# Performance work log

Hardware: AMD Instinct MI355X
Metric: run time of the kernel (lower is better)

## Reference

```python
import math
import jax, jax.numpy as jnp
from jax import lax
import numpy as np

LN_EPS = 1e-5
K = 3          # deform-conv kernel size
PAD = 1        # 'same' padding so offset map matches output resolution


def setup_inputs() -> dict:
    key = jax.random.key(0)
    ks = jax.random.split(key, 6)
    B, C, H, W, Co = 4, 256, 64, 64, 256
    x = jax.random.normal(ks[0], (B, C, H, W), jnp.float32)
    dwc_w = jax.random.normal(ks[1], (C, 1, K, K), jnp.float32) * 0.02
    ln_w = jnp.ones((C,), jnp.float32)
    ln_b = jnp.zeros((C,), jnp.float32)
    fcd_w = jax.random.normal(ks[2], (1, C, 1, 1), jnp.float32) * 0.02
    fca_w = jax.random.normal(ks[3], (1, C, 1, 1), jnp.float32) * 0.02
    fan_in = C * K * K
    dconv_w = jax.random.normal(ks[4], (Co, C, K, K), jnp.float32) / math.sqrt(fan_in)
    dconv_b = jnp.zeros((Co,), jnp.float32)
    return dict(x=x, dwc_w=dwc_w, ln_w=ln_w, ln_b=ln_b,
                fcd_w=fcd_w, fca_w=fca_w, dconv_w=dconv_w, dconv_b=dconv_b)


def _bilinear_sample(x, py, px):
    # x: [B,C,H,W]; py/px: [B,KK,H,W] float sample positions (zero-padded border)
    B, C, H, W = x.shape
    y0 = jnp.floor(py); x0 = jnp.floor(px)
    y1 = y0 + 1.0;      x1 = x0 + 1.0
    wy1 = py - y0; wy0 = 1.0 - wy1
    wx1 = px - x0; wx0 = 1.0 - wx1

    def gather(yy, xx):
        valid = ((yy >= 0) & (yy < H) & (xx >= 0) & (xx < W)).astype(x.dtype)
        iy = jnp.clip(yy, 0, H - 1).astype(jnp.int32)
        ix = jnp.clip(xx, 0, W - 1).astype(jnp.int32)
        # per-batch fancy gather -> [B,C,KK,H,W]
        v = jax.vmap(lambda img, a, b: img[:, a, b])(x, iy, ix)
        return v * valid[:, None]

    return (gather(y0, x0) * (wy0 * wx0)[:, None]
          + gather(y0, x1) * (wy0 * wx1)[:, None]
          + gather(y1, x0) * (wy1 * wx0)[:, None]
          + gather(y1, x1) * (wy1 * wx1)[:, None])


def reference(x, dwc_w, ln_w, ln_b, fcd_w, fca_w, dconv_w, dconv_b):
    B, C, H, W = x.shape
    KK = K * K
    # --- offset branch ---
    h = lax.conv_general_dilated(x, dwc_w, (1, 1), ((1, 1), (1, 1)),
                                 dimension_numbers=('NCHW', 'OIHW', 'NCHW'),
                                 feature_group_count=C)
    mu = h.mean(axis=1, keepdims=True)
    var = h.var(axis=1, keepdims=True)
    h = (h - mu) * lax.rsqrt(var + LN_EPS)
    h = h * ln_w[None, :, None, None] + ln_b[None, :, None, None]
    h = jax.nn.relu(h)
    r = jax.nn.relu(jnp.einsum('bchw,oc->bohw', h, fcd_w[:, :, 0, 0]))      # [B,1,H,W]
    t = jnp.einsum('bchw,oc->bohw', h, fca_w[:, :, 0, 0])
    theta = (t / (1.0 + jnp.abs(t))) * (math.pi / 180.0)                     # softsign * pi/180
    ox = r * jnp.cos(theta)
    oy = r * jnp.sin(theta)
    # torch code: offsets = cat([ox tiled KK, oy tiled KK], dim=1) -> [B,2KK,H,W]
    off = jnp.concatenate([jnp.tile(ox, (1, KK, 1, 1)), jnp.tile(oy, (1, KK, 1, 1))], axis=1)
    # torchvision DeformConv2d convention: channel 2k = dy, channel 2k+1 = dx
    dy = off[:, 0::2]   # [B,KK,H,W]
    dx = off[:, 1::2]
    # --- deformable sampling ---
    ky = jnp.repeat(jnp.arange(K), K).astype(x.dtype)   # kernel row per tap
    kx = jnp.tile(jnp.arange(K), K).astype(x.dtype)     # kernel col per tap
    py = (jnp.arange(H, dtype=x.dtype) - PAD)[None, None, :, None] + ky[None, :, None, None] + dy
    px = (jnp.arange(W, dtype=x.dtype) - PAD)[None, None, None, :] + kx[None, :, None, None] + dx
    sampled = _bilinear_sample(x, py, px)               # [B,C,KK,H,W]
    Co = dconv_w.shape[0]
    out = jnp.einsum('bckhw,ock->bohw', sampled, dconv_w.reshape(Co, C, KK))
    return out + dconv_b[None, :, None, None]
```

## Files before the change

### kernel.cpp

```cpp
#include <hip/hip_runtime.h>
#include <hip/hip_bf16.h>

#define B_   4
#define C_   256
#define CO_  256
#define H_   64
#define W_   64
#define HW_  4096

typedef __attribute__((ext_vector_type(8))) short short8;
typedef __attribute__((ext_vector_type(4))) float f32x4;
typedef __attribute__((ext_vector_type(2))) float f32x2;

static __device__ __forceinline__ unsigned short f2bf(float f) {
    unsigned u = __builtin_bit_cast(unsigned, f);
    unsigned r = (u + 0x7fffu + ((u >> 16) & 1u)) >> 16;
    return (unsigned short)r;
}
static __device__ __forceinline__ f32x2 pk_mul(f32x2 a, f32x2 b) {
    f32x2 d; asm("v_pk_mul_f32 %0, %1, %2" : "=v"(d) : "v"(a), "v"(b)); return d;
}
static __device__ __forceinline__ f32x2 pk_fma(f32x2 a, f32x2 b, f32x2 c) {
    f32x2 d; asm("v_pk_fma_f32 %0, %1, %2, %3" : "=v"(d) : "v"(a), "v"(b), "v"(c)); return d;
}
static __device__ __forceinline__ f32x2 pk_add(f32x2 a, f32x2 b) {
    f32x2 d; asm("v_pk_add_f32 %0, %1, %2" : "=v"(d) : "v"(a), "v"(b)); return d;
}
static __device__ __forceinline__ unsigned cvtpk(float a, float b) {
    unsigned r; asm("v_cvt_pk_bf16_f32 %0, %1, %2" : "=v"(r) : "v"(a), "v"(b)); return r;
}
static __device__ __forceinline__ f32x2 unpack_bf2(unsigned d) {
    f32x2 v;
    v.x = __builtin_bit_cast(float, d << 16);
    v.y = __builtin_bit_cast(float, d & 0xffff0000u);
    return v;
}

__global__ void k_pre(const float* __restrict__ x, unsigned short* __restrict__ xT,
                      const float* __restrict__ w, unsigned short* __restrict__ Bt,
                      const float* __restrict__ dwc_w, float* __restrict__ dwcT)
{
    int bid = blockIdx.x;
    int tid = threadIdx.x;
    if (bid < 1024) {
        __shared__ float t[32][132];
        int b   = bid >> 8;
        int rem = bid & 255;
        int hwT = rem >> 1, cT = rem & 1;
        int hw0 = hwT * 32, c0 = cT * 128;
        const float* src = x + (size_t)b * C_ * HW_;
        {
            int hw4 = (tid & 7) << 2;
            int cr  = tid >> 3;
#pragma unroll
            for (int it = 0; it < 4; ++it) {
                int c = cr + it * 32;
                f32x4 v = *(const f32x4*)(src + (size_t)(c0 + c) * HW_ + hw0 + hw4);
                t[hw4 + 0][c] = v.x;
                t[hw4 + 1][c] = v.y;
                t[hw4 + 2][c] = v.z;
                t[hw4 + 3][c] = v.w;
            }
        }
        __syncthreads();
        {
            int c8  = (tid & 15) << 3;
            int hwr = tid >> 4;
            unsigned short* dst = xT + (size_t)(((b << 12) + hw0) * 256) + c0 + c8;
#pragma unroll
            for (int it = 0; it < 2; ++it) {
                int hw = hwr + it * 16;
                f32x4 va = *(const f32x4*)&t[hw][c8];
                f32x4 vb = *(const f32x4*)&t[hw][c8 + 4];
                uint4 u;
                u.x = cvtpk(va.x, va.y);
                u.y = cvtpk(va.z, va.w);
                u.z = cvtpk(vb.x, vb.y);
                u.w = cvtpk(vb.z, vb.w);
                *(uint4*)(dst + (size_t)hw * 256) = u;
            }
        }
    } else {
        int pb = bid - 1024;
        if (pb < 9) dwcT[pb * 256 + tid] = dwc_w[tid * 9 + pb];
        int e = pb * 256 + tid;
        int j   = e & 7;
        int l4  = (e >> 3) & 3;
        int l15 = (e >> 5) & 15;
        int ks  = (e >> 9) & 7;
        int og  = (e >> 12) & 15;
        int k   = e >> 16;
        int o = og * 16 + l15;
        int c = ks * 32 + l4 * 8 + j;
        Bt[e] = f2bf(w[(o * C_ + c) * 9 + k]);
    }
}

__global__ void k_offsets(const unsigned short* __restrict__ xT,
                          const float* __restrict__ dwcT,
                          const float* __restrict__ ln_w,
                          const float* __restrict__ ln_b,
                          const float* __restrict__ fcd_w,
                          const float* __restrict__ fca_w,
                          float* __restrict__ OX, float* __restrict__ OY)
{
    int tid = threadIdx.x;
    int bi = blockIdx.x;
    int g = ((bi & 7) << 6) | (bi >> 3);
    int p0 = g << 5;
    int b = p0 >> 12;
    int y = (p0 >> 6) & 63;
    int xh = p0 & 63;
    int gpos = tid >> 4;
    int csub = tid & 15;
    int ch0 = csub << 4;
    const unsigned short* xb = xT + (size_t)b * HW_ * C_;

    f32x2 acc2[8];
#pragma unroll
    for (int i = 0; i < 8; ++i) { acc2[i].x = 0.f; acc2[i].y = 0.f; }
#pragma unroll
    for (int j = 0; j < 9; ++j) {
        int gy = y + j / 3 - 1, gx = xh + gpos + j % 3 - 1;
        if (gy >= 0 && gy < H_ && gx >= 0 && gx < W_) {
            const unsigned short* p = xb + (size_t)((gy << 6) + gx) * 256 + ch0;
            short8 rlo = *(const short8*)(p);
            short8 rhi = *(const short8*)(p + 8);
            const float* wrow = dwcT + j * 256 + ch0;
#pragma unroll
            for (int q = 0; q < 4; ++q) {
                f32x4 wv = *(const f32x4*)(wrow + q * 4);
                f32x2 w01v; w01v.x = wv.x; w01v.y = wv.y;
                f32x2 w23v; w23v.x = wv.z; w23v.y = wv.w;
                unsigned lo = (q < 2) ? ((unsigned*)&rlo)[q * 2] : ((unsigned*)&rhi)[(q - 2) * 2];
                unsigned hi = (q < 2) ? ((unsigned*)&rlo)[q * 2 + 1] : ((unsigned*)&rhi)[(q - 2) * 2 + 1];
                acc2[q * 2 + 0] = pk_fma(unpack_bf2(lo), w01v, acc2[q * 2 + 0]);
                acc2[q * 2 + 1] = pk_fma(unpack_bf2(hi), w23v, acc2[q * 2 + 1]);
            }
        }
    }
    f32x2 sum2, sq2;
    sum2.x = 0.f; sum2.y = 0.f; sq2.x = 0.f; sq2.y = 0.f;
#pragma unroll
    for (int i = 0; i < 8; ++i) {
        sum2 = pk_add(sum2, acc2[i]);
        sq2  = pk_fma(acc2[i], acc2[i], sq2);
    }
    float s1 = sum2.x + sum2.y, s2 = sq2.x + sq2.y;
#pragma unroll
    for (int m = 1; m <= 8; m <<= 1) {
        s1 += __shfl_xor(s1, m);
        s2 += __shfl_xor(s2, m);
    }
    float mu  = s1 * (1.f / 256.f);
    float var = s2 * (1.f / 256.f) - mu * mu;
    float rs  = rsqrtf(var + 1e-5f);
    float d1 = 0.f, d2 = 0.f;
#pragma unroll
    for (int q = 0; q < 4; ++q) {
        f32x4 lwv = *(const f32x4*)(ln_w  + ch0 + q * 4);
        f32x4 lbv = *(const f32x4*)(ln_b  + ch0 + q * 4);
        f32x4 fdv = *(const f32x4*)(fcd_w + ch0 + q * 4);
        f32x4 fav = *(const f32x4*)(fca_w + ch0 + q * 4);
#pragma unroll
        for (int i = 0; i < 4; ++i) {
            float av = (i & 1) ? acc2[q * 2 + (i >> 1)].y : acc2[q * 2 + (i >> 1)].x;
            float hn = (av - mu) * rs * lwv[i] + lbv[i];
            hn = fmaxf(hn, 0.f);
            d1 = fmaf(hn, fdv[i], d1);
            d2 = fmaf(hn, fav[i], d2);
        }
    }
#pragma unroll
    for (int m = 1; m <= 8; m <<= 1) {
        d1 += __shfl_xor(d1, m);
        d2 += __shfl_xor(d2, m);
    }
    if (csub == 0) {
        float r0 = fmaxf(d1, 0.f);
        float theta = d2 / (1.f + fabsf(d2)) * 0.017453292519943295f;
        int pos = p0 + gpos;
        OX[pos] = r0 * cosf(theta);
        OY[pos] = r0 * sinf(theta);
    }
}

__launch_bounds__(1024, 8)
__global__ void k_main(const unsigned short* __restrict__ xT,
                       const float* __restrict__ OX, const float* __restrict__ OY,
                       const unsigned short* __restrict__ Bt,
                       const float* __restrict__ bias,
                       float* __restrict__ out)
{
    __shared__ __align__(16) unsigned char smem[32768];

    int tid = threadIdx.x;
    int bi = blockIdx.x;
    int g = ((bi & 7) << 6) | (bi >> 3);
    int p0 = g << 5;
    int b = p0 >> 12;
    int y = (p0 >> 6) & 63;
    int xh = p0 & 63;

    int lane = tid & 63, wid = tid >> 6;
    int l15 = lane & 15, l4 = lane >> 4;

    f32x4 acc[2];
#pragma unroll
    for (int m = 0; m < 2; ++m) {
        acc[m].x = 0.f; acc[m].y = 0.f; acc[m].z = 0.f; acc[m].w = 0.f;
    }

    int gpos = tid >> 5;
    unsigned csub = (unsigned)tid & 31u;
    const char* xbB = (const char*)(xT + (size_t)b * HW_ * C_);
    const unsigned short* bwave = Bt + (unsigned)wid * 4096u
                                     + (unsigned)(l15 * 32 + l4 * 8);
    unsigned rowb = (unsigned)gpos * 512u;
    unsigned wsl  = (csub ^ ((unsigned)gpos & 15u)) << 4;
    float ox = OX[p0 + gpos], oy = OY[p0 + gpos];

    unsigned o00, o01, o10, o11;
    f32x2 W00, W01, W10, W11;

#define GADDR(k)                                                                  \
    {   int ky = (k) / 3, kx = (k) - ky * 3;                                      \
        float dyv = ((k) <= 4) ? ox : oy;                                         \
        float dxv = ((k) <= 3) ? ox : oy;                                         \
        float py = (float)(y - 1 + ky) + dyv;                                     \
        float px = (float)(xh + gpos - 1 + kx) + dxv;                             \
        float y0f = floorf(py), x0f = floorf(px);                                 \
        int y0 = (int)y0f, x0 = (int)x0f;                                         \
        int y1 = y0 + 1, x1 = x0 + 1;                                             \
        float wy1 = py - y0f, wy0 = 1.f - wy1;                                    \
        float wx1 = px - x0f, wx0 = 1.f - wx1;                                    \
        float vy0 = (y0 >= 0 && y0 < H_) ? 1.f : 0.f;                             \
        float vy1 = (y1 >= 0 && y1 < H_) ? 1.f : 0.f;                             \
        float vx0 = (x0 >= 0 && x0 < W_) ? 1.f : 0.f;                             \
        float vx1 = (x1 >= 0 && x1 < W_) ? 1.f : 0.f;                             \
        float w00 = wy0 * wx0 * vy0 * vx0, w01 = wy0 * wx1 * vy0 * vx1;           \
        float w10 = wy1 * wx0 * vy1 * vx0, w11 = wy1 * wx1 * vy1 * vx1;           \
        W00.x = w00; W00.y = w00; W01.x = w01; W01.y = w01;                       \
        W10.x = w10; W10.y = w10; W11.x = w11; W11.y = w11;                       \
        int y0c = min(max(y0, 0), H_ - 1), y1c = min(max(y1, 0), H_ - 1);         \
        int x0c = min(max(x0, 0), W_ - 1), x1c = min(max(x1, 0), W_ - 1);         \
        unsigned cb = csub << 4;                                                  \
        o00 = (unsigned)((y0c << 6) + x0c) * 512u + cb;                           \
        o01 = (unsigned)((y0c << 6) + x1c) * 512u + cb;                           \
        o10 = (unsigned)((y1c << 6) + x0c) * 512u + cb;                           \
        o11 = (unsigned)((y1c << 6) + x1c) * 512u + cb;                           \
    }

#define GATHER_TAP(hbase)                                                         \
    {   short8 r00 = *(const short8*)(xbB + o00);                                 \
        short8 r01 = *(const short8*)(xbB + o01);                                 \
        short8 r10 = *(const short8*)(xbB + o10);                                 \
        short8 r11 = *(const short8*)(xbB + o11);                                 \
        uint4 pkv;                                                                \
        _Pragma("unroll")                                                         \
        for (int dw = 0; dw < 4; ++dw) {                                          \
            f32x2 a2 = pk_mul(unpack_bf2(((unsigned*)&r00)[dw]), W00);            \
            a2 = pk_fma(unpack_bf2(((unsigned*)&r01)[dw]), W01, a2);              \
            a2 = pk_fma(unpack_bf2(((unsigned*)&r10)[dw]), W10, a2);              \
            a2 = pk_fma(unpack_bf2(((unsigned*)&r11)[dw]), W11, a2);              \
            ((unsigned*)&pkv)[dw] = cvtpk(a2.x, a2.y);                            \
        }                                                                         \
        *(uint4*)(smem + (hbase) + rowb + wsl) = pkv;                             \
    }

#define MFMA_TAP(k, hbase)                                                        \
    {   const unsigned short* bk = bwave + (unsigned)(k) * 65536u;                \
        _Pragma("unroll")                                                         \
        for (int ks = 0; ks < 8; ++ks) {                                          \
            short8 bf = *(const short8*)(bk + ks * 512);                          \
            unsigned sl = ((unsigned)(ks * 4 + l4) ^ (unsigned)l15) << 4;         \
            _Pragma("unroll")                                                     \
            for (int mf = 0; mf < 2; ++mf) {                                      \
                unsigned row = (unsigned)(mf * 16 + l15);                         \
                short8 a = *(const short8*)(smem + (hbase) + row * 512u + sl);    \
                acc[mf] = __builtin_amdgcn_mfma_f32_16x16x32_bf16(a, bf, acc[mf], 0, 0, 0); \
            }                                                                     \
        }                                                                         \
    }

    GADDR(0);
    GATHER_TAP(0u);
    __syncthreads();

#pragma unroll
    for (int k = 0; k < 9; ++k) {
        unsigned cur = (k & 1) ? 16384u : 0u;
        unsigned nxt = (k & 1) ? 0u : 16384u;
        if (k < 8) {
            GADDR(k + 1);
            GATHER_TAP(nxt);
        }
        MFMA_TAP(k, cur);
        __syncthreads();
    }

    int col = wid * 16 + l15;
    float bv = bias[col];
    float* obase = out + ((size_t)(b * CO_ + col)) * HW_ + (y << 6) + xh;
#pragma unroll
    for (int mf = 0; mf < 2; ++mf) {
        f32x4 v;
        v.x = acc[mf].x + bv;
        v.y = acc[mf].y + bv;
        v.z = acc[mf].z + bv;
        v.w = acc[mf].w + bv;
        *(f32x4*)(obase + mf * 16 + l4 * 4) = v;
    }
}

extern "C" void kernel_launch(void* const* d_in, const int* in_sizes, int n_in,
                              void* d_out, int out_size, void* d_ws, size_t ws_size,
                              hipStream_t stream) {
    const float* x      = (const float*)d_in[0];
    const float* dwc_w  = (const float*)d_in[1];
    const float* ln_w   = (const float*)d_in[2];
    const float* ln_b   = (const float*)d_in[3];
    const float* fcd_w  = (const float*)d_in[4];
    const float* fca_w  = (const float*)d_in[5];
    const float* dconv_w= (const float*)d_in[6];
    const float* dconv_b= (const float*)d_in[7];
    float* out = (float*)d_out;

    unsigned char* ws = (unsigned char*)d_ws;
    unsigned short* xT = (unsigned short*)(ws);
    unsigned short* Bt = (unsigned short*)(ws + 8388608);
    float* dwcT        = (float*)(ws + 9568256);
    float* OX          = (float*)(ws + 9577472);
    float* OY          = (float*)(ws + 9643008);

    k_pre<<<3328, 256, 0, stream>>>(x, xT, dconv_w, Bt, dwc_w, dwcT);
    k_offsets<<<512, 512, 0, stream>>>(xT, dwcT, ln_w, ln_b, fcd_w, fca_w, OX, OY);
    k_main<<<512, 1024, 0, stream>>>(xT, OX, OY, Bt, dconv_b, out);
}
```

Before: 80.25 us.

## Split output channels across two 256-thread blocks with 2x2 MFMA register tiles

```diff
diff --git a/kernel.cpp b/kernel.cpp
--- a/kernel.cpp
+++ b/kernel.cpp
@@ -185,7 +185,7 @@
     }
 }
 
-__launch_bounds__(1024, 8)
+__launch_bounds__(256, 4)
 __global__ void k_main(const unsigned short* __restrict__ xT,
                        const float* __restrict__ OX, const float* __restrict__ OY,
                        const unsigned short* __restrict__ Bt,
@@ -196,8 +196,10 @@
 
     int tid = threadIdx.x;
     int bi = blockIdx.x;
-    int g = ((bi & 7) << 6) | (bi >> 3);
-    int p0 = g << 5;
+    int g = ((bi & 7) << 7) | (bi >> 3);
+    int tile = g >> 1;
+    int n0g = g & 1;
+    int p0 = tile << 5;
     int b = p0 >> 12;
     int y = (p0 >> 6) & 63;
     int xh = p0 & 63;
@@ -205,19 +207,20 @@
     int lane = tid & 63, wid = tid >> 6;
     int l15 = lane & 15, l4 = lane >> 4;
 
-    f32x4 acc[2];
-#pragma unroll
-    for (int m = 0; m < 2; ++m) {
-        acc[m].x = 0.f; acc[m].y = 0.f; acc[m].z = 0.f; acc[m].w = 0.f;
-    }
-
-    int gpos = tid >> 5;
-    unsigned csub = (unsigned)tid & 31u;
+    f32x4 acc[2][2];
+#pragma unroll
+    for (int m = 0; m < 2; ++m)
+#pragma unroll
+        for (int n = 0; n < 2; ++n) {
+            acc[m][n].x = 0.f; acc[m][n].y = 0.f; acc[m][n].z = 0.f; acc[m][n].w = 0.f;
+        }
+
+    int gpos = tid >> 3;
+    unsigned csub = (unsigned)tid & 7u;
     const char* xbB = (const char*)(xT + (size_t)b * HW_ * C_);
-    const unsigned short* bwave = Bt + (unsigned)wid * 4096u
+    const unsigned short* bwave = Bt + (unsigned)(n0g * 8 + wid * 2) * 4096u
                                      + (unsigned)(l15 * 32 + l4 * 8);
     unsigned rowb = (unsigned)gpos * 512u;
-    unsigned wsl  = (csub ^ ((unsigned)gpos & 15u)) << 4;
     float ox = OX[p0 + gpos], oy = OY[p0 + gpos];
 
     unsigned o00, o01, o10, o11;
@@ -252,34 +255,40 @@
     }
 
 #define GATHER_TAP(hbase)                                                         \
-    {   short8 r00 = *(const short8*)(xbB + o00);                                 \
-        short8 r01 = *(const short8*)(xbB + o01);                                 \
-        short8 r10 = *(const short8*)(xbB + o10);                                 \
-        short8 r11 = *(const short8*)(xbB + o11);                                 \
-        uint4 pkv;                                                                \
-        _Pragma("unroll")                                                         \
-        for (int dw = 0; dw < 4; ++dw) {                                          \
-            f32x2 a2 = pk_mul(unpack_bf2(((unsigned*)&r00)[dw]), W00);            \
-            a2 = pk_fma(unpack_bf2(((unsigned*)&r01)[dw]), W01, a2);              \
-            a2 = pk_fma(unpack_bf2(((unsigned*)&r10)[dw]), W10, a2);              \
-            a2 = pk_fma(unpack_bf2(((unsigned*)&r11)[dw]), W11, a2);              \
-            ((unsigned*)&pkv)[dw] = cvtpk(a2.x, a2.y);                            \
+    {   _Pragma("unroll")                                                         \
+        for (int cq = 0; cq < 4; ++cq) {                                          \
+            unsigned gb = (unsigned)cq * 128u;                                    \
+            short8 r00 = *(const short8*)(xbB + o00 + gb);                        \
+            short8 r01 = *(const short8*)(xbB + o01 + gb);                        \
+            short8 r10 = *(const short8*)(xbB + o10 + gb);                        \
+            short8 r11 = *(const short8*)(xbB + o11 + gb);                        \
+            uint4 pkv;                                                            \
+            _Pragma("unroll")                                                     \
+            for (int dw = 0; dw < 4; ++dw) {                                      \
+                f32x2 a2 = pk_mul(unpack_bf2(((unsigned*)&r00)[dw]), W00);        \
+                a2 = pk_fma(unpack_bf2(((unsigned*)&r01)[dw]), W01, a2);          \
+                a2 = pk_fma(unpack_bf2(((unsigned*)&r10)[dw]), W10, a2);          \
+                a2 = pk_fma(unpack_bf2(((unsigned*)&r11)[dw]), W11, a2);          \
+                ((unsigned*)&pkv)[dw] = cvtpk(a2.x, a2.y);                        \
+            }                                                                     \
+            unsigned slot = ((unsigned)cq * 8u + csub) ^ ((unsigned)gpos & 7u);   \
+            *(uint4*)(smem + (hbase) + rowb + slot * 16u) = pkv;                  \
         }                                                                         \
-        *(uint4*)(smem + (hbase) + rowb + wsl) = pkv;                             \
     }
 
 #define MFMA_TAP(k, hbase)                                                        \
     {   const unsigned short* bk = bwave + (unsigned)(k) * 65536u;                \
         _Pragma("unroll")                                                         \
         for (int ks = 0; ks < 8; ++ks) {                                          \
-            short8 bf = *(const short8*)(bk + ks * 512);                          \
-            unsigned sl = ((unsigned)(ks * 4 + l4) ^ (unsigned)l15) << 4;         \
-            _Pragma("unroll")                                                     \
-            for (int mf = 0; mf < 2; ++mf) {                                      \
-                unsigned row = (unsigned)(mf * 16 + l15);                         \
-                short8 a = *(const short8*)(smem + (hbase) + row * 512u + sl);    \
-                acc[mf] = __builtin_amdgcn_mfma_f32_16x16x32_bf16(a, bf, acc[mf], 0, 0, 0); \
-            }                                                                     \
+            short8 bf0 = *(const short8*)(bk + ks * 512);                         \
+            short8 bf1 = *(const short8*)(bk + 4096 + ks * 512);                  \
+            unsigned sl = ((unsigned)(ks * 4 + l4) ^ ((unsigned)l15 & 7u)) << 4;  \
+            short8 a0 = *(const short8*)(smem + (hbase) + (unsigned)l15 * 512u + sl);        \
+            short8 a1 = *(const short8*)(smem + (hbase) + (unsigned)(16 + l15) * 512u + sl); \
+            acc[0][0] = __builtin_amdgcn_mfma_f32_16x16x32_bf16(a0, bf0, acc[0][0], 0, 0, 0); \
+            acc[0][1] = __builtin_amdgcn_mfma_f32_16x16x32_bf16(a0, bf1, acc[0][1], 0, 0, 0); \
+            acc[1][0] = __builtin_amdgcn_mfma_f32_16x16x32_bf16(a1, bf0, acc[1][0], 0, 0, 0); \
+            acc[1][1] = __builtin_amdgcn_mfma_f32_16x16x32_bf16(a1, bf1, acc[1][1], 0, 0, 0); \
         }                                                                         \
     }
 
@@ -299,17 +308,20 @@
         __syncthreads();
     }
 
-    int col = wid * 16 + l15;
-    float bv = bias[col];
-    float* obase = out + ((size_t)(b * CO_ + col)) * HW_ + (y << 6) + xh;
-#pragma unroll
-    for (int mf = 0; mf < 2; ++mf) {
-        f32x4 v;
-        v.x = acc[mf].x + bv;
-        v.y = acc[mf].y + bv;
-        v.z = acc[mf].z + bv;
-        v.w = acc[mf].w + bv;
-        *(f32x4*)(obase + mf * 16 + l4 * 4) = v;
+#pragma unroll
+    for (int nf = 0; nf < 2; ++nf) {
+        int col = n0g * 128 + wid * 32 + nf * 16 + l15;
+        float bv = bias[col];
+        float* obase = out + ((size_t)(b * CO_ + col)) * HW_ + (y << 6) + xh;
+#pragma unroll
+        for (int mf = 0; mf < 2; ++mf) {
+            f32x4 v;
+            v.x = acc[mf][nf].x + bv;
+            v.y = acc[mf][nf].y + bv;
+            v.z = acc[mf][nf].z + bv;
+            v.w = acc[mf][nf].w + bv;
+            *(f32x4*)(obase + mf * 16 + l4 * 4) = v;
+        }
     }
 }
 
@@ -335,5 +347,5 @@
 
     k_pre<<<3328, 256, 0, stream>>>(x, xT, dconv_w, Bt, dwc_w, dwcT);
     k_offsets<<<512, 512, 0, stream>>>(xT, dwcT, ln_w, ln_b, fcd_w, fca_w, OX, OY);
-    k_main<<<512, 1024, 0, stream>>>(xT, OX, OY, Bt, dconv_b, out);
-}
+    k_main<<<1024, 256, 0, stream>>>(xT, OX, OY, Bt, dconv_b, out);
+}
```

Measured after the change: 82.84 us. 1.03x slower.
